# Kernel tuning notes

Measured on AMD Instinct MI355X. Metric: run time of the kernel, lower is better.

## Reference

```python
import jax, jax.numpy as jnp
import numpy as np

B, S, D_IN, D_OUT = 4, 2048, 1024, 1024


def setup_inputs() -> dict:
    key = jax.random.key(0)
    k1, k2, k3, k4 = jax.random.split(key, 4)
    x = jax.random.normal(k1, (B, S, D_IN), dtype=jnp.float32)
    scale = 1.0 / np.sqrt(D_IN)
    Wq = jax.random.normal(k2, (D_IN, D_OUT), dtype=jnp.float32) * scale
    Wk = jax.random.normal(k3, (D_IN, D_OUT), dtype=jnp.float32) * scale
    Wv = jax.random.normal(k4, (D_IN, D_OUT), dtype=jnp.float32) * scale
    return {"x": x, "Wq": Wq, "Wk": Wk, "Wv": Wv}


def reference(x, Wq, Wk, Wv):
    # QKV projections (Linear, no bias)
    q = jnp.einsum('bsd,de->bse', x, Wq)  # [B,S,D_OUT]
    k = jnp.einsum('bsd,de->bse', x, Wk)
    v = jnp.einsum('bsd,de->bse', x, Wv)
    d_out = Wq.shape[1]
    # raw scores [B,S,S], scaled after masking (identical math: -inf stays -inf)
    scores = jnp.einsum('bqe,bke->bqk', q, k) * (d_out ** -0.5)
    S_ = x.shape[1]
    # causal mask: future positions (j > i) are masked out
    causal = jnp.triu(jnp.ones((S_, S_), dtype=bool), k=1)
    scores = jnp.where(causal[None, :, :], -jnp.inf, scores)
    attn = jax.nn.softmax(scores, axis=-1)  # dropout p=0.0 -> identity
    return jnp.einsum('bqk,bke->bqe', attn, v)
```

## Files before the change

kernel.cpp:

```cpp
#include <hip/hip_runtime.h>
#include <stdint.h>

typedef unsigned short u16;
typedef unsigned int u32;
typedef __bf16 bf16x8 __attribute__((ext_vector_type(8)));
typedef float f32x4 __attribute__((ext_vector_type(4)));

#define BM 128
#define BN 128
#define BK 64

__device__ __forceinline__ u16 f2bf(float x) {
  union { float f; uint32_t u; } c; c.f = x;
  uint32_t r = (c.u + 0x7FFFu + ((c.u >> 16) & 1u)) >> 16;
  return (u16)r;
}
__device__ __forceinline__ float bf2f(u16 v) {
  union { uint32_t u; float f; } c; c.u = ((uint32_t)v) << 16;
  return c.f;
}

__device__ __forceinline__ void async_copy16(const u16* g, u16* l) {
  __builtin_amdgcn_global_load_lds(
      (const __attribute__((address_space(1))) void*)g,
      (__attribute__((address_space(3))) void*)l,
      16, 0, 0);
}

__global__ void zerofill_u16(u16* __restrict__ p) {
  long i = (long)blockIdx.x * 256 + threadIdx.x;
  p[i] = 0;
}

__global__ __launch_bounds__(256)
void prep(const void* __restrict__ xs, const void* __restrict__ w0,
          const void* __restrict__ w1, const void* __restrict__ w2,
          u16* __restrict__ xn, u16* __restrict__ WT3, u32* __restrict__ flag,
          float* __restrict__ sigma, int nxb)
{
  __shared__ int sh_hits;
  __shared__ u16 tile[64][72];
  if (threadIdx.x == 0) sh_hits = 0;
  __syncthreads();
  {
    const u16* w = (const u16*)w0;
    int h = 0;
    for (int i = threadIdx.x; i < 8192; i += 256)
      if ((w[i] & 0x7F80u) == 0x7F80u) h++;
    if (h) atomicAdd(&sh_hits, h);
  }
  __syncthreads();
  const bool isf32 = (sh_hits > 0);
  const int blk = blockIdx.x;
  const int tid = threadIdx.x;
  if (blk == 0 && tid == 0) *flag = isf32 ? 1000u : 0u;

  if (blk < nxb) {
    long i = ((long)blk * 256 + tid) * 8;
    u16 o[8];
    if (isf32) {
      const float* s = (const float*)xs + i;
      f32x4 a = *(const f32x4*)s;
      f32x4 b = *(const f32x4*)(s + 4);
#pragma unroll
      for (int c = 0; c < 4; ++c) { o[c] = f2bf(a[c]); o[c + 4] = f2bf(b[c]); }
    } else {
      *(uint4*)o = *(const uint4*)((const u16*)xs + i);
    }
    *(uint4*)(xn + i) = *(uint4*)o;
  } else if (blk < nxb + 768) {
    const int Dd = 1024;
    int t = blk - nxb;
    int z = t >> 8;
    int r = t & 255;
    const int r0 = (r >> 4) * 64, c0 = (r & 15) * 64;
    const void* src = (z == 0) ? w0 : (z == 1) ? w1 : w2;
    u16* out = WT3 + (long)z * Dd * Dd;
#pragma unroll
    for (int p = 0; p < 2; ++p) {
      int v = tid + p * 256;
      int row = v >> 3, c8 = (v & 7) * 8;
      u16 tt[8];
      if (isf32) {
        const float* sp = (const float*)src + (long)(r0 + row) * Dd + c0 + c8;
        f32x4 a = *(const f32x4*)sp;
        f32x4 b = *(const f32x4*)(sp + 4);
#pragma unroll
        for (int c = 0; c < 4; ++c) { tt[c] = f2bf(a[c]); tt[c + 4] = f2bf(b[c]); }
      } else {
        *(uint4*)tt = *(const uint4*)((const u16*)src + (long)(r0 + row) * Dd + c0 + c8);
      }
#pragma unroll
      for (int c = 0; c < 8; ++c) tile[row][c8 + c] = tt[c];
    }
    __syncthreads();
#pragma unroll
    for (int p = 0; p < 2; ++p) {
      int v = tid + p * 256;
      int oc = v >> 3, r8 = (v & 7) * 8;
      union { uint4 q; u16 s[8]; } tt;
#pragma unroll
      for (int c = 0; c < 8; ++c) tt.s[c] = tile[r8 + c][oc];
      *(uint4*)(out + (long)(c0 + oc) * Dd + r0 + r8) = tt.q;
    }
  } else {
    int t = blk - (nxb + 768);
    *(f32x4*)(sigma + ((long)t * 256 + tid) * 4) = f32x4{0.f, 0.f, 0.f, 0.f};
  }
}

template <int MODE>
__global__ __launch_bounds__(256, 4)
void gemm_nt(const u16* __restrict__ A, const u16* __restrict__ B, void* __restrict__ Cv,
             const u32* __restrict__ flag, float* __restrict__ sigma, int sigStride,
             int K, int lda, int ldb, int ldc,
             long sA, long sB, long sC, long cOff,
             float scale, int trik, int ntri,
             const u16* __restrict__ vSrc, u16* __restrict__ vtDst,
             long sV, long sVT, int ldV, int ldVT)
{
  __shared__ u16 As[BM * BK];
  __shared__ u16 Bs[BN * BK];
  const int bz = blockIdx.z;
  const int tid = threadIdx.x;

  int bm, bn;
  if constexpr (MODE == 3) {
    if ((int)blockIdx.x >= ntri) {
      int t2 = blockIdx.x - ntri;
      const u16* in = vSrc + (long)bz * sV;
      u16* out = vtDst + (long)bz * sVT;
      const int c0 = (t2 & 15) * 64;
      const int r0 = (t2 >> 4) * 64;
      u16 (*tile)[72] = reinterpret_cast<u16(*)[72]>(As);
#pragma unroll
      for (int p = 0; p < 2; ++p) {
        int v = tid + p * 256;
        int row = v >> 3, c8 = (v & 7) * 8;
        union { uint4 q; u16 s[8]; } t;
        t.q = *(const uint4*)(in + (long)(r0 + row) * ldV + c0 + c8);
#pragma unroll
        for (int i = 0; i < 8; ++i) tile[row][c8 + i] = t.s[i];
      }
      __syncthreads();
#pragma unroll
      for (int p = 0; p < 2; ++p) {
        int v = tid + p * 256;
        int oc = v >> 3, r8 = (v & 7) * 8;
        union { uint4 q; u16 s[8]; } t;
#pragma unroll
        for (int i = 0; i < 8; ++i) t.s[i] = tile[r8 + i][oc];
        *(uint4*)(out + (long)(c0 + oc) * ldVT + r0 + r8) = t.q;
      }
      return;
    }
    {
      const int t = blockIdx.x;
      const int cum[11] = {0, 10, 26, 36, 52, 68, 78, 94, 110, 126, 136};
      const int ssm[10] = {0, 1, 1, 2, 2, 2, 3, 3, 3, 3};
      const int ssn[10] = {0, 0, 1, 0, 1, 2, 0, 1, 2, 3};
      int s = 0;
      while (cum[s + 1] <= t) ++s;
      const int l = t - cum[s];
      const int sm = ssm[s], sn = ssn[s];
      int tm, tn;
      if (sm == sn) {
        tm = 0;
        while ((tm + 1) * (tm + 2) / 2 <= l) ++tm;
        tn = l - tm * (tm + 1) / 2;
      } else { tm = l >> 2; tn = l & 3; }
      bm = sm * 4 + tm;
      bn = sn * 4 + tn;
    }
  } else {
    bm = blockIdx.y;
    if (trik) bm = gridDim.y - 1 - bm;
    bn = blockIdx.x;
  }

  A += (long)bz * sA;
  B += (long)bz * sB;

  const int wid  = tid >> 6;
  const int lane = tid & 63;
  const int l16  = lane & 15;
  const int lk   = lane >> 4;
  const int srow = lane >> 3;
  const int swz  = ((lane & 7) ^ srow) * 8;
  const int m0 = bm * BM, n0 = bn * BN;

  int nk = K / BK;
  if (trik) { int lim = (m0 + BM) / BK; if (lim < nk) nk = lim; }

  f32x4 acc[4][4] = {};

  for (int kt = 0; kt < nk; ++kt) {
    const int k0 = kt * BK;
#pragma unroll
    for (int c = 0; c < 4; ++c) {
      const int rb = wid * 32 + c * 8;
      async_copy16(A + (long)(m0 + rb + srow) * lda + (k0 + swz), As + rb * BK);
      async_copy16(B + (long)(n0 + rb + srow) * ldb + (k0 + swz), Bs + rb * BK);
    }
    __syncthreads();
#pragma unroll
    for (int kh = 0; kh < 2; ++kh) {
      bf16x8 av[4], bv[4];
#pragma unroll
      for (int i = 0; i < 4; ++i) {
        const int Ra = (wid >> 1) * 64 + i * 16 + l16;
        const int Rb = (wid & 1)  * 64 + i * 16 + l16;
        const int ca = ((kh * 4 + lk) ^ (l16 & 7)) * 8;
        av[i] = *(const bf16x8*)(As + Ra * BK + ca);
        bv[i] = *(const bf16x8*)(Bs + Rb * BK + ca);
      }
#pragma unroll
      for (int mi = 0; mi < 4; ++mi)
#pragma unroll
        for (int ni = 0; ni < 4; ++ni)
          acc[mi][ni] = __builtin_amdgcn_mfma_f32_16x16x32_bf16(av[mi], bv[ni], acc[mi][ni], 0, 0, 0);
    }
    __syncthreads();
  }

  const int rb0 = m0 + (wid >> 1) * 64;
  const int cb0 = n0 + (wid & 1) * 64;
  const long cbase = (long)bz * sC + cOff;

  if constexpr (MODE == 3) {
    u16* Cp = (u16*)Cv;
    const bool diag = (bm == bn);
    float* sig = sigma + (long)bz * sigStride;
#pragma unroll
    for (int mi = 0; mi < 4; ++mi)
#pragma unroll
      for (int r = 0; r < 4; ++r) {
        const int row = rb0 + mi * 16 + lk * 4 + r;
        float part = 0.f;
#pragma unroll
        for (int ni = 0; ni < 4; ++ni) {
          const int col = cb0 + ni * 16 + l16;
          float ev = __expf(acc[mi][ni][r] * scale);
          if (diag && col > row) ev = 0.f;
          u16 b = f2bf(ev);
          part += bf2f(b);
          Cp[cbase + (long)row * ldc + col] = b;
        }
#pragma unroll
        for (int o = 1; o < 16; o <<= 1) part += __shfl_xor(part, o);
        if (l16 == 0) atomicAdd(&sig[row], part);
      }
  } else {
    const bool f32out = (MODE == 2) && (*flag > 32);
    const float* sig = (MODE == 2) ? (sigma + (long)bz * sigStride) : nullptr;
#pragma unroll
    for (int mi = 0; mi < 4; ++mi)
#pragma unroll
      for (int r = 0; r < 4; ++r) {
        const int row = rb0 + mi * 16 + lk * 4 + r;
        float rs = scale;
        if constexpr (MODE == 2) rs = 1.0f / sig[row];
#pragma unroll
        for (int ni = 0; ni < 4; ++ni) {
          const int col = cb0 + ni * 16 + l16;
          const float v = acc[mi][ni][r] * rs;
          const long idx = cbase + (long)row * ldc + col;
          if constexpr (MODE == 0) {
            ((u16*)Cv)[idx] = f2bf(v);
          } else {
            if (f32out) ((float*)Cv)[idx] = v;
            else        ((u16*)Cv)[idx]   = f2bf(v);
          }
        }
      }
  }
}

extern "C" void kernel_launch(void* const* d_in, const int* in_sizes, int n_in,
                              void* d_out, int out_size, void* d_ws, size_t ws_size,
                              hipStream_t stream)
{
  (void)in_sizes; (void)n_in; (void)out_size;
  const int Bb = 4, S = 2048, D = 1024, D3 = 3072;
  const long SD  = (long)S * D;
  const long SD3 = (long)S * D3;
  const long SS  = (long)S * S;
  const long N_X = (long)Bb * SD;
  const long N_W = (long)D * D;
  const int NTRI = 16 * 17 / 2;

  char* ws = (char*)d_ws;
  size_t off = 0;
  auto take = [&](size_t bytes) -> void* {
    void* p = ws + off;
    off = (off + bytes + 255) & ~((size_t)255);
    return p;
  };

  u32*   flag  = (u32*)take(4096);
  float* sigma = (float*)take((size_t)Bb * S * 4);
  u16*   xn    = (u16*)take((size_t)N_X * 2);
  u16*   WT3   = (u16*)take((size_t)3 * N_W * 2);
  const size_t off_common = off;

  const size_t needA = off_common + (size_t)(N_X * 3 * 2)
                     + (size_t)(N_X * 2)
                     + (size_t)(Bb * SS * 2) + 4096;
  const size_t needC = off_common + (size_t)(S * (long)D3 * 2)
                     + (size_t)(SD * 2)
                     + (size_t)(SS * 2) + 4096;

  if (ws_size < needC) {
    zerofill_u16<<<(int)(N_X / 256), 256, 0, stream>>>((u16*)d_out);
    return;
  }

  const int nxb = (int)(N_X / 2048);
  prep<<<nxb + 768 + 8, 256, 0, stream>>>(d_in[0], d_in[1], d_in[2], d_in[3],
                                          xn, WT3, flag, sigma, nxb);

  const float scl = 0.03125f;

  if (ws_size >= needA) {
    u16* QKV = (u16*)take((size_t)N_X * 3 * 2);
    u16* VT  = (u16*)take((size_t)N_X * 2);
    u16* E   = (u16*)take((size_t)Bb * SS * 2);

    gemm_nt<0><<<dim3(D3 / BN, (int)(N_X / D) / BM, 1), 256, 0, stream>>>(
        xn, WT3, QKV, flag, nullptr, 0, D, D, D, D3,
        0, 0, 0, 0, 1.f, 0, 0, nullptr, nullptr, 0, 0, 0, 0);

    gemm_nt<3><<<dim3(NTRI + 512, 1, Bb), 256, 0, stream>>>(
        QKV, QKV + 1024, E, flag, sigma, S, D, D3, D3, S,
        SD3, SD3, SS, 0, scl, 0, NTRI,
        QKV + 2048, VT, SD3, SD, D3, S);

    gemm_nt<2><<<dim3(D / BN, S / BM, Bb), 256, 0, stream>>>(
        E, VT, d_out, flag, sigma, S, S, S, S, D,
        SS, SD, SD, 0, 1.f, 1, 0, nullptr, nullptr, 0, 0, 0, 0);
  } else {
    u16* QKVb = (u16*)take((size_t)S * D3 * 2);
    u16* VTb  = (u16*)take((size_t)SD * 2);
    u16* Eb   = (u16*)take((size_t)SS * 2);

    for (int b = 0; b < Bb; ++b) {
      gemm_nt<0><<<dim3(D3 / BN, S / BM, 1), 256, 0, stream>>>(
          xn + (long)b * SD, WT3, QKVb, flag, nullptr, 0, D, D, D, D3,
          0, 0, 0, 0, 1.f, 0, 0, nullptr, nullptr, 0, 0, 0, 0);

      gemm_nt<3><<<dim3(NTRI + 512, 1, 1), 256, 0, stream>>>(
          QKVb, QKVb + 1024, Eb, flag, sigma + (long)b * S, S, D, D3, D3, S,
          0, 0, 0, 0, scl, 0, NTRI,
          QKVb + 2048, VTb, 0, 0, D3, S);

      gemm_nt<2><<<dim3(D / BN, S / BM, 1), 256, 0, stream>>>(
          Eb, VTb, d_out, flag, sigma + (long)b * S, S, S, S, S, D,
          0, 0, 0, (long)b * SD, 1.f, 1, 0, nullptr, nullptr, 0, 0, 0, 0);
    }
  }
}
```

Before: 245.8 us.

## Add dedicated 256x128 triple-buffered QKV projection GEMM kernel

Replaces the generic gemm_nt<0> QKV projection with a specialized kernel using 512-thread blocks, 256x128 output tiles, a 3-stage async global-to-LDS pipeline with XOR-swizzled LDS layout and raised wave priority around the MFMA block. The aim is more data reuse per block and better overlap of loads with MFMA work in the largest GEMM. It drops the flag/sigma handling of the generic path and hardcodes K=1024 (NK=16). The epilogue writes scalar bf16 stores, which may be less efficient than vectorized stores.

```diff
diff --git a/kernel.cpp b/kernel.cpp
--- a/kernel.cpp
+++ b/kernel.cpp
@@ -107,6 +107,86 @@
     int t = blk - (nxb + 768);
     *(f32x4*)(sigma + ((long)t * 256 + tid) * 4) = f32x4{0.f, 0.f, 0.f, 0.f};
   }
+}
+
+__global__ __launch_bounds__(512, 2)
+void gemm_qkv(const u16* __restrict__ A, const u16* __restrict__ B,
+              u16* __restrict__ C, int lda, int ldb, int ldc)
+{
+  __shared__ u16 ldsq[3 * 24576];
+  const int tid  = threadIdx.x;
+  const int wid  = tid >> 6;
+  const int lane = tid & 63;
+  const int l16  = lane & 15;
+  const int lk   = lane >> 4;
+  const int srow = lane >> 3;
+  const int swz  = ((lane & 7) ^ srow) * 8;
+  const int wr   = wid >> 1, wc = wid & 1;
+  const int m0 = blockIdx.y * 256, n0 = blockIdx.x * 128;
+
+  const u16* gA = A + (long)(m0 + wid * 32 + srow) * lda + swz;
+  const u16* gB = B + (long)(n0 + wid * 16 + srow) * ldb + swz;
+
+  const int NK = 16;
+
+  auto issue = [&](int kt) {
+    u16* Ab = ldsq + (kt % 3) * 24576;
+    u16* Bb = Ab + 16384;
+    const int k0 = kt * 64;
+#pragma unroll
+    for (int c = 0; c < 4; ++c)
+      async_copy16(gA + (long)(c * 8) * lda + k0, Ab + (wid * 32 + c * 8) * 64);
+#pragma unroll
+    for (int c = 0; c < 2; ++c)
+      async_copy16(gB + (long)(c * 8) * ldb + k0, Bb + (wid * 16 + c * 8) * 64);
+  };
+
+  f32x4 acc[4][4] = {};
+  issue(0);
+  issue(1);
+
+#pragma unroll
+  for (int kt = 0; kt < NK; ++kt) {
+    if (kt < NK - 1) asm volatile("s_waitcnt vmcnt(6) lgkmcnt(0)" ::: "memory");
+    else             asm volatile("s_waitcnt vmcnt(0) lgkmcnt(0)" ::: "memory");
+    asm volatile("s_barrier" ::: "memory");
+    if (kt + 2 < NK) issue(kt + 2);
+    const u16* Ab = ldsq + (kt % 3) * 24576;
+    const u16* Bb = Ab + 16384;
+#pragma unroll
+    for (int kh = 0; kh < 2; ++kh) {
+      bf16x8 av[4], bv[4];
+#pragma unroll
+      for (int i = 0; i < 4; ++i) {
+        const int Ra = wr * 64 + i * 16 + l16;
+        const int Rb = wc * 64 + i * 16 + l16;
+        const int ca = ((kh * 4 + lk) ^ (l16 & 7)) * 8;
+        av[i] = *(const bf16x8*)(Ab + Ra * 64 + ca);
+        bv[i] = *(const bf16x8*)(Bb + Rb * 64 + ca);
+      }
+      __builtin_amdgcn_s_setprio(1);
+#pragma unroll
+      for (int mi = 0; mi < 4; ++mi)
+#pragma unroll
+        for (int ni = 0; ni < 4; ++ni)
+          acc[mi][ni] = __builtin_amdgcn_mfma_f32_16x16x32_bf16(av[mi], bv[ni], acc[mi][ni], 0, 0, 0);
+      __builtin_amdgcn_s_setprio(0);
+    }
+  }
+
+  const int rb0 = m0 + wr * 64;
+  const int cb0 = n0 + wc * 64;
+#pragma unroll
+  for (int mi = 0; mi < 4; ++mi)
+#pragma unroll
+    for (int r = 0; r < 4; ++r) {
+      const int row = rb0 + mi * 16 + lk * 4 + r;
+#pragma unroll
+      for (int ni = 0; ni < 4; ++ni) {
+        const int col = cb0 + ni * 16 + l16;
+        C[(long)row * ldc + col] = f2bf(acc[mi][ni][r]);
+      }
+    }
 }
 
 template <int MODE>
@@ -326,9 +406,8 @@
     u16* VT  = (u16*)take((size_t)N_X * 2);
     u16* E   = (u16*)take((size_t)Bb * SS * 2);
 
-    gemm_nt<0><<<dim3(D3 / BN, (int)(N_X / D) / BM, 1), 256, 0, stream>>>(
-        xn, WT3, QKV, flag, nullptr, 0, D, D, D, D3,
-        0, 0, 0, 0, 1.f, 0, 0, nullptr, nullptr, 0, 0, 0, 0);
+    gemm_qkv<<<dim3(D3 / 128, (int)(N_X / D) / 256, 1), 512, 0, stream>>>(
+        xn, WT3, QKV, D, D, D3);
 
     gemm_nt<3><<<dim3(NTRI + 512, 1, Bb), 256, 0, stream>>>(
         QKV, QKV + 1024, E, flag, sigma, S, D, D3, D3, S,
@@ -344,9 +423,8 @@
     u16* Eb   = (u16*)take((size_t)SS * 2);
 
     for (int b = 0; b < Bb; ++b) {
-      gemm_nt<0><<<dim3(D3 / BN, S / BM, 1), 256, 0, stream>>>(
-          xn + (long)b * SD, WT3, QKVb, flag, nullptr, 0, D, D, D, D3,
-          0, 0, 0, 0, 1.f, 0, 0, nullptr, nullptr, 0, 0, 0, 0);
+      gemm_qkv<<<dim3(D3 / 128, S / 256, 1), 512, 0, stream>>>(
+          xn + (long)b * SD, WT3, QKVb, D, D, D3);
 
       gemm_nt<3><<<dim3(NTRI + 512, 1, 1), 256, 0, stream>>>(
           QKVb, QKVb + 1024, Eb, flag, sigma + (long)b * S, S, D, D3, D3, S,
```

Measured after the change: 247.1 us. About the same (+0.5%).

## Compute V transposed directly via swapped-operand GEMM instead of transposing V

Applied to the files above, without the earlier changes.

V is now produced directly in transposed layout by a new GEMM mode that multiplies Wv^T by x and scatters columns into per-batch VT buffers. The QK projection GEMM shrinks to two thirds of its width, and the transpose blocks are removed from the score kernel. This drops the write and reread of V plus the separate transpose pass, at the cost of one extra kernel launch and strided bf16 stores in the new mode.

```diff
diff --git a/kernel.cpp b/kernel.cpp
--- a/kernel.cpp
+++ b/kernel.cpp
@@ -115,9 +115,7 @@
              const u32* __restrict__ flag, float* __restrict__ sigma, int sigStride,
              int K, int lda, int ldb, int ldc,
              long sA, long sB, long sC, long cOff,
-             float scale, int trik, int ntri,
-             const u16* __restrict__ vSrc, u16* __restrict__ vtDst,
-             long sV, long sVT, int ldV, int ldVT)
+             float scale, int trik, int ntri)
 {
   __shared__ u16 As[BM * BK];
   __shared__ u16 Bs[BN * BK];
@@ -126,52 +124,23 @@
 
   int bm, bn;
   if constexpr (MODE == 3) {
-    if ((int)blockIdx.x >= ntri) {
-      int t2 = blockIdx.x - ntri;
-      const u16* in = vSrc + (long)bz * sV;
-      u16* out = vtDst + (long)bz * sVT;
-      const int c0 = (t2 & 15) * 64;
-      const int r0 = (t2 >> 4) * 64;
-      u16 (*tile)[72] = reinterpret_cast<u16(*)[72]>(As);
-#pragma unroll
-      for (int p = 0; p < 2; ++p) {
-        int v = tid + p * 256;
-        int row = v >> 3, c8 = (v & 7) * 8;
-        union { uint4 q; u16 s[8]; } t;
-        t.q = *(const uint4*)(in + (long)(r0 + row) * ldV + c0 + c8);
-#pragma unroll
-        for (int i = 0; i < 8; ++i) tile[row][c8 + i] = t.s[i];
-      }
-      __syncthreads();
-#pragma unroll
-      for (int p = 0; p < 2; ++p) {
-        int v = tid + p * 256;
-        int oc = v >> 3, r8 = (v & 7) * 8;
-        union { uint4 q; u16 s[8]; } t;
-#pragma unroll
-        for (int i = 0; i < 8; ++i) t.s[i] = tile[r8 + i][oc];
-        *(uint4*)(out + (long)(c0 + oc) * ldVT + r0 + r8) = t.q;
-      }
-      return;
-    }
-    {
-      const int t = blockIdx.x;
-      const int cum[11] = {0, 10, 26, 36, 52, 68, 78, 94, 110, 126, 136};
-      const int ssm[10] = {0, 1, 1, 2, 2, 2, 3, 3, 3, 3};
-      const int ssn[10] = {0, 0, 1, 0, 1, 2, 0, 1, 2, 3};
-      int s = 0;
-      while (cum[s + 1] <= t) ++s;
-      const int l = t - cum[s];
-      const int sm = ssm[s], sn = ssn[s];
-      int tm, tn;
-      if (sm == sn) {
-        tm = 0;
-        while ((tm + 1) * (tm + 2) / 2 <= l) ++tm;
-        tn = l - tm * (tm + 1) / 2;
-      } else { tm = l >> 2; tn = l & 3; }
-      bm = sm * 4 + tm;
-      bn = sn * 4 + tn;
-    }
+    const int t = blockIdx.x;
+    const int cum[11] = {0, 10, 26, 36, 52, 68, 78, 94, 110, 126, 136};
+    const int ssm[10] = {0, 1, 1, 2, 2, 2, 3, 3, 3, 3};
+    const int ssn[10] = {0, 0, 1, 0, 1, 2, 0, 1, 2, 3};
+    int s = 0;
+    while (cum[s + 1] <= t) ++s;
+    const int l = t - cum[s];
+    const int sm = ssm[s], sn = ssn[s];
+    int tm, tn;
+    if (sm == sn) {
+      tm = 0;
+      while ((tm + 1) * (tm + 2) / 2 <= l) ++tm;
+      tn = l - tm * (tm + 1) / 2;
+    } else { tm = l >> 2; tn = l & 3; }
+    bm = sm * 4 + tm;
+    bn = sn * 4 + tn;
+    (void)ntri;
   } else {
     bm = blockIdx.y;
     if (trik) bm = gridDim.y - 1 - bm;
@@ -249,6 +218,20 @@
 #pragma unroll
         for (int o = 1; o < 16; o <<= 1) part += __shfl_xor(part, o);
         if (l16 == 0) atomicAdd(&sig[row], part);
+      }
+  } else if constexpr (MODE == 4) {
+    u16* Cp = (u16*)Cv;
+#pragma unroll
+    for (int mi = 0; mi < 4; ++mi)
+#pragma unroll
+      for (int r = 0; r < 4; ++r) {
+        const int row = rb0 + mi * 16 + lk * 4 + r;
+#pragma unroll
+        for (int ni = 0; ni < 4; ++ni) {
+          const int col = cb0 + ni * 16 + l16;
+          const long idx = (long)row * ldc + (long)(col >> 11) * sC + (col & 2047);
+          Cp[idx] = f2bf(acc[mi][ni][r]);
+        }
       }
   } else {
     const bool f32out = (MODE == 2) && (*flag > 32);
@@ -281,9 +264,9 @@
                               hipStream_t stream)
 {
   (void)in_sizes; (void)n_in; (void)out_size;
-  const int Bb = 4, S = 2048, D = 1024, D3 = 3072;
+  const int Bb = 4, S = 2048, D = 1024, D2 = 2048;
   const long SD  = (long)S * D;
-  const long SD3 = (long)S * D3;
+  const long SD2 = (long)S * D2;
   const long SS  = (long)S * S;
   const long N_X = (long)Bb * SD;
   const long N_W = (long)D * D;
@@ -303,10 +286,10 @@
   u16*   WT3   = (u16*)take((size_t)3 * N_W * 2);
   const size_t off_common = off;
 
-  const size_t needA = off_common + (size_t)(N_X * 3 * 2)
+  const size_t needA = off_common + (size_t)(Bb * SD2 * 2)
                      + (size_t)(N_X * 2)
                      + (size_t)(Bb * SS * 2) + 4096;
-  const size_t needC = off_common + (size_t)(S * (long)D3 * 2)
+  const size_t needC = off_common + (size_t)(SD2 * 2)
                      + (size_t)(SD * 2)
                      + (size_t)(SS * 2) + 4096;
 
@@ -322,40 +305,46 @@
   const float scl = 0.03125f;
 
   if (ws_size >= needA) {
-    u16* QKV = (u16*)take((size_t)N_X * 3 * 2);
-    u16* VT  = (u16*)take((size_t)N_X * 2);
-    u16* E   = (u16*)take((size_t)Bb * SS * 2);
-
-    gemm_nt<0><<<dim3(D3 / BN, (int)(N_X / D) / BM, 1), 256, 0, stream>>>(
-        xn, WT3, QKV, flag, nullptr, 0, D, D, D, D3,
-        0, 0, 0, 0, 1.f, 0, 0, nullptr, nullptr, 0, 0, 0, 0);
-
-    gemm_nt<3><<<dim3(NTRI + 512, 1, Bb), 256, 0, stream>>>(
-        QKV, QKV + 1024, E, flag, sigma, S, D, D3, D3, S,
-        SD3, SD3, SS, 0, scl, 0, NTRI,
-        QKV + 2048, VT, SD3, SD, D3, S);
+    u16* QK = (u16*)take((size_t)Bb * SD2 * 2);
+    u16* VT = (u16*)take((size_t)N_X * 2);
+    u16* E  = (u16*)take((size_t)Bb * SS * 2);
+
+    gemm_nt<0><<<dim3(D2 / BN, (int)(N_X / D) / BM, 1), 256, 0, stream>>>(
+        xn, WT3, QK, flag, nullptr, 0, D, D, D, D2,
+        0, 0, 0, 0, 1.f, 0, 0);
+
+    gemm_nt<4><<<dim3((int)(N_X / D) / BN, D / BM, 1), 256, 0, stream>>>(
+        WT3 + 2 * N_W, xn, VT, flag, nullptr, 0, D, D, D, S,
+        0, 0, SD, 0, 1.f, 0, 0);
+
+    gemm_nt<3><<<dim3(NTRI, 1, Bb), 256, 0, stream>>>(
+        QK, QK + 1024, E, flag, sigma, S, D, D2, D2, S,
+        SD2, SD2, SS, 0, scl, 0, NTRI);
 
     gemm_nt<2><<<dim3(D / BN, S / BM, Bb), 256, 0, stream>>>(
         E, VT, d_out, flag, sigma, S, S, S, S, D,
-        SS, SD, SD, 0, 1.f, 1, 0, nullptr, nullptr, 0, 0, 0, 0);
+        SS, SD, SD, 0, 1.f, 1, 0);
   } else {
-    u16* QKVb = (u16*)take((size_t)S * D3 * 2);
-    u16* VTb  = (u16*)take((size_t)SD * 2);
-    u16* Eb   = (u16*)take((size_t)SS * 2);
+    u16* QKb = (u16*)take((size_t)SD2 * 2);
+    u16* VTb = (u16*)take((size_t)SD * 2);
+    u16* Eb  = (u16*)take((size_t)SS * 2);
 
     for (int b = 0; b < Bb; ++b) {
-      gemm_nt<0><<<dim3(D3 / BN, S / BM, 1), 256, 0, stream>>>(
-          xn + (long)b * SD, WT3, QKVb, flag, nullptr, 0, D, D, D, D3,
-          0, 0, 0, 0, 1.f, 0, 0, nullptr, nullptr, 0, 0, 0, 0);
-
-      gemm_nt<3><<<dim3(NTRI + 512, 1, 1), 256, 0, stream>>>(
-          QKVb, QKVb + 1024, Eb, flag, sigma + (long)b * S, S, D, D3, D3, S,
-          0, 0, 0, 0, scl, 0, NTRI,
-          QKVb + 2048, VTb, 0, 0, D3, S);
+      gemm_nt<0><<<dim3(D2 / BN, S / BM, 1), 256, 0, stream>>>(
+          xn + (long)b * SD, WT3, QKb, flag, nullptr, 0, D, D, D, D2,
+          0, 0, 0, 0, 1.f, 0, 0);
+
+      gemm_nt<4><<<dim3(S / BN, D / BM, 1), 256, 0, stream>>>(
+          WT3 + 2 * N_W, xn + (long)b * SD, VTb, flag, nullptr, 0, D, D, D, S,
+          0, 0, 0, 0, 1.f, 0, 0);
+
+      gemm_nt<3><<<dim3(NTRI, 1, 1), 256, 0, stream>>>(
+          QKb, QKb + 1024, Eb, flag, sigma + (long)b * S, S, D, D2, D2, S,
+          0, 0, 0, 0, scl, 0, NTRI);
 
       gemm_nt<2><<<dim3(D / BN, S / BM, 1), 256, 0, stream>>>(
           Eb, VTb, d_out, flag, sigma + (long)b * S, S, S, S, S, D,
-          0, 0, 0, (long)b * SD, 1.f, 1, 0, nullptr, nullptr, 0, 0, 0, 0);
-    }
-  }
-}
+          0, 0, 0, (long)b * SD, 1.f, 1, 0);
+    }
+  }
+}
```

New measurement: 246.9 us. About the same (+0.5%).
